# Kernel optimization log

Hardware: AMD Instinct MI355X
Metric: run time of the kernel (lower is better)

## Reference

```python
import jax, jax.numpy as jnp
import numpy as np

B, L = 128, 64000
FS, STEP, NFILT, HID, HID2, OUT = 256, 200, 64, 512, 512, 10


def _ilin(lb, ub, W, b=0.0):
    # interval affine: center/radius form
    c = (lb + ub) * 0.5
    r = (ub - lb) * 0.5
    oc = c @ W + b
    orr = r @ jnp.abs(W)
    return oc - orr, oc + orr


def _imul(al, au, bl, bu):
    # interval product: extremes over 4 corner products
    p = jnp.stack([al * bl, al * bu, au * bl, au * bu])
    return p.min(axis=0), p.max(axis=0)


def _cell(xl, xu, hl, hu, cl, cu, wih, whh, bias):
    # interval LSTM cell, torch gate order i,f,g,o
    gl1, gu1 = _ilin(xl, xu, wih)
    gl2, gu2 = _ilin(hl, hu, whh)
    gl = gl1 + gl2 + bias
    gu = gu1 + gu2 + bias
    il, fl, ggl, ol = jnp.split(gl, 4, axis=-1)
    iu, fu, ggu, ou = jnp.split(gu, 4, axis=-1)
    il, iu = jax.nn.sigmoid(il), jax.nn.sigmoid(iu)
    fl, fu = jax.nn.sigmoid(fl), jax.nn.sigmoid(fu)
    ggl, ggu = jnp.tanh(ggl), jnp.tanh(ggu)
    fcl, fcu = _imul(fl, fu, cl, cu)
    igl, igu = _imul(il, iu, ggl, ggu)
    ncl, ncu = fcl + igl, fcu + igu
    nhl, nhu = _imul(jax.nn.sigmoid(ol), jax.nn.sigmoid(ou), jnp.tanh(ncl), jnp.tanh(ncu))
    return nhl, nhu, ncl, ncu


def setup_inputs() -> dict:
    key = jax.random.key(0)
    ks = jax.random.split(key, 13)
    x = 0.1 * jax.random.normal(ks[0], (B, L), jnp.float32)
    eps = 0.01
    s = 0.3  # keep LSTM gates out of saturation
    return {
        "input_lb": x - eps,
        "input_ub": x + eps,
        "mtx1": jax.random.normal(ks[1], (FS, FS + 2), jnp.float32) / np.float32(np.sqrt(FS)),
        "mtx2": jax.random.uniform(ks[2], (FS + 2, NFILT), jnp.float32) / np.float32(FS + 2),
        "lin1_w": jax.random.normal(ks[3], (NFILT, HID), jnp.float32) / np.float32(np.sqrt(NFILT)),
        "lin1_b": 0.01 * jax.random.normal(ks[4], (HID,), jnp.float32),
        "w_ih0": s * jax.random.normal(ks[5], (HID, 4 * HID2), jnp.float32) / np.float32(np.sqrt(HID)),
        "w_hh0": s * jax.random.normal(ks[6], (HID2, 4 * HID2), jnp.float32) / np.float32(np.sqrt(HID2)),
        "b0": 0.01 * jax.random.normal(ks[7], (4 * HID2,), jnp.float32),
        "w_ih1": s * jax.random.normal(ks[8], (HID2, 4 * HID2), jnp.float32) / np.float32(np.sqrt(HID2)),
        "w_hh1": s * jax.random.normal(ks[9], (HID2, 4 * HID2), jnp.float32) / np.float32(np.sqrt(HID2)),
        "b1": 0.01 * jax.random.normal(ks[10], (4 * HID2,), jnp.float32),
        "lin2_w": jax.random.normal(ks[11], (HID2, OUT), jnp.float32) / np.float32(np.sqrt(HID2)),
        "lin2_b": 0.01 * jax.random.normal(ks[12], (OUT,), jnp.float32),
    }


def reference(input_lb, input_ub, mtx1, mtx2, lin1_w, lin1_b,
              w_ih0, w_hh0, b0, w_ih1, w_hh1, b1, lin2_w, lin2_b):
    Bc, Lc = input_lb.shape
    pad = jnp.zeros((Bc, STEP), input_lb.dtype)
    lb = jnp.concatenate([input_lb, pad], axis=1)
    ub = jnp.concatenate([input_ub, pad], axis=1)
    Lp = Lc + STEP
    F = (Lp - FS - 1) // STEP + 1  # frames with i + FS < Lp (break condition)
    idx = jnp.arange(F)[:, None] * STEP + jnp.arange(FS)[None, :]  # [F, FS]
    flb, fub = lb[:, idx], ub[:, idx]  # [B, F, FS]
    # pre-LSTM interval chain, vectorized over all frames
    l1l, l1u = _ilin(flb, fub, mtx1)  # [B, F, FS+2]
    a, b = l1l * l1l, l1u * l1u
    squ = jnp.maximum(a, b)
    sql = jnp.where((l1l <= 0) & (l1u >= 0), 0.0, jnp.minimum(a, b))
    l2l, l2u = _ilin(sql, squ, mtx2, 1e-10)  # mtx2 >= 0, inputs >= 0 -> lb > 0
    lgl, lgu = jnp.log(l2l), jnp.log(l2u)
    n1l, n1u = _ilin(lgl, lgu, lin1_w, lin1_b)  # [B, F, HID]
    rl, ru = jnp.maximum(n1l, 0.0), jnp.maximum(n1u, 0.0)

    H2 = w_hh0.shape[0]
    z = jnp.zeros((Bc, H2), input_lb.dtype)

    def step(carry, xs):
        h0l, h0u, c0l, c0u, h1l, h1u, c1l, c1u = carry
        xl, xu = xs
        h0l, h0u, c0l, c0u = _cell(xl, xu, h0l, h0u, c0l, c0u, w_ih0, w_hh0, b0)
        h1l, h1u, c1l, c1u = _cell(h0l, h0u, h1l, h1u, c1l, c1u, w_ih1, w_hh1, b1)
        return (h0l, h0u, c0l, c0u, h1l, h1u, c1l, c1u), None

    carry, _ = jax.lax.scan(step, (z,) * 8,
                            (jnp.swapaxes(rl, 0, 1), jnp.swapaxes(ru, 0, 1)))
    h1l, h1u = carry[4], carry[5]  # last frame, top LSTM layer
    ol, ou = _ilin(h1l, h1u, lin2_w, lin2_b)
    return jnp.stack([ol, ou])  # [2, B, OUT] logit bounds
```

## Files before the change

kernel.cpp:

```cpp
#include <hip/hip_runtime.h>
#include <hip/hip_bf16.h>
#include <math.h>

#define BATCH 128
#define LEN   64000
#define FS    256
#define STEPS 200
#define NFILT 64
#define HID   512
#define HID2  512
#define NOUT  10
#define NF    320
#define G4    2048
#define KTOT  1024
#define NBLK  256
#define HSLOT (BATCH * HID2)

typedef __bf16  bf16x8 __attribute__((ext_vector_type(8)));
typedef float   f32x4  __attribute__((ext_vector_type(4)));
typedef __hip_bfloat16 hbf;

#define ARV(b)  (128 + (b) * 16)
#define REL_(i) (128 + 4096 + (i) * 16)
#define BAR_WORDS (128 + 4096 + 128)

__device__ __forceinline__ float fsig(float x) { return 1.f / (1.f + __expf(-x)); }
__device__ __forceinline__ float ftanh(float x) { return 1.f - 2.f / (__expf(2.f * x) + 1.f); }
__device__ __forceinline__ void imulf_(float al, float au, float bl, float bu,
                                       float& lo, float& hi) {
    const float p1 = al * bl, p2 = al * bu, p3 = au * bl, p4 = au * bu;
    lo = fminf(fminf(p1, p2), fminf(p3, p4));
    hi = fmaxf(fmaxf(p1, p2), fmaxf(p3, p4));
}

__device__ __forceinline__ bf16x8 loadA16_agent(const hbf* p) {
    union { unsigned long long u[2]; bf16x8 v; } t;
    unsigned long long* q = (unsigned long long*)p;
    t.u[0] = __hip_atomic_load(q,     __ATOMIC_RELAXED, __HIP_MEMORY_SCOPE_AGENT);
    t.u[1] = __hip_atomic_load(q + 1, __ATOMIC_RELAXED, __HIP_MEMORY_SCOPE_AGENT);
    return t.v;
}
__device__ __forceinline__ unsigned ld_flag(const unsigned* p) {
    return __hip_atomic_load(p, __ATOMIC_RELAXED, __HIP_MEMORY_SCOPE_AGENT);
}
__device__ __forceinline__ void st_flag(unsigned* p, unsigned v) {
    __hip_atomic_store(p, v, __ATOMIC_RELAXED, __HIP_MEMORY_SCOPE_AGENT);
}

__global__ __launch_bounds__(256) void prep_weights_kernel(
    const float* __restrict__ wih, const float* __restrict__ whh,
    hbf* __restrict__ Wt)
{
    __shared__ float tile[32][33];
    const int n0 = blockIdx.x * 32;
    const int k0 = blockIdx.y * 32;
    const int tx = threadIdx.x & 31;
    const int ty = threadIdx.x >> 5;

    for (int r = ty; r < 32; r += 8) {
        const int k = k0 + r;
        const float* src = (k < HID) ? (wih + (size_t)k * G4)
                                     : (whh + (size_t)(k - HID) * G4);
        tile[r][tx] = src[n0 + tx];
    }
    __syncthreads();
    for (int r = ty; r < 32; r += 8) {
        const int n = n0 + r;
        Wt[(size_t)n * KTOT + k0 + tx] = __float2bfloat16(tile[tx][r]);
    }
}

__global__ __launch_bounds__(256) void prep_mtx1_kernel(
    const float* __restrict__ mtx1, hbf* __restrict__ W)
{
    __shared__ float tile[32][33];
    const int n0 = blockIdx.x * 32;
    const int k0 = blockIdx.y * 32;
    const int tx = threadIdx.x & 31;
    const int ty = threadIdx.x >> 5;

    for (int r = ty; r < 32; r += 8) {
        const int k = k0 + r;
        const int n = n0 + tx;
        tile[r][tx] = (n < FS + 2) ? mtx1[k * (FS + 2) + n] : 0.f;
    }
    __syncthreads();
    for (int r = ty; r < 32; r += 8) {
        const int n = n0 + r;
        if (n < 272)
            W[(size_t)n * 256 + k0 + tx] = __float2bfloat16(tile[tx][r]);
    }
}

__global__ __launch_bounds__(256) void prep_lin1_kernel(
    const float* __restrict__ lin1_w, hbf* __restrict__ W)
{
    __shared__ float tile[32][33];
    const int n0 = blockIdx.x * 32;
    const int k0 = blockIdx.y * 32;
    const int tx = threadIdx.x & 31;
    const int ty = threadIdx.x >> 5;

    for (int r = ty; r < 32; r += 8)
        tile[r][tx] = lin1_w[(size_t)(k0 + r) * HID + n0 + tx];
    __syncthreads();
    for (int r = ty; r < 32; r += 8)
        W[(size_t)(n0 + r) * 64 + k0 + tx] = __float2bfloat16(tile[tx][r]);
}

#define FB_A1C  0
#define FB_A1R  8704
#define FB_O1C  17408
#define FB_O1R  34816
#define FB_S3C  52224
#define FB_S3R  54272
#define FB_SIZE 56320

__global__ __launch_bounds__(512) void frontend3_kernel(
    const float* __restrict__ lb, const float* __restrict__ ub,
    const hbf* __restrict__ Wt1f,
    const float* __restrict__ mtx2,
    const hbf* __restrict__ Wt3f,
    const float* __restrict__ lin1_b,
    hbf* __restrict__ Xc, hbf* __restrict__ Xr)
{
    __shared__ char fbuf[FB_SIZE];
    hbf*   A1c = (hbf*)(fbuf + FB_A1C);
    hbf*   A1r = (hbf*)(fbuf + FB_A1R);
    float* o1C = (float*)(fbuf + FB_O1C);
    float* o1R = (float*)(fbuf + FB_O1R);
    hbf*   SQL = A1c;
    hbf*   SQU = A1r;
    hbf*   s3c = (hbf*)(fbuf + FB_S3C);
    hbf*   s3r = (hbf*)(fbuf + FB_S3R);

    const int tid  = threadIdx.x;
    const int row0 = blockIdx.x * 16;
    const int b    = row0 / NF;
    const int f0   = row0 % NF;

    for (int c = tid; c < 16 * 256; c += 512) {
        const int m = c >> 8, i = c & 255;
        const int pos = (f0 + m) * STEPS + i;
        float l = 0.f, u = 0.f;
        if (pos < LEN) {
            l = lb[(size_t)b * LEN + pos];
            u = ub[(size_t)b * LEN + pos];
        }
        A1c[m * 272 + i] = __float2bfloat16(0.5f * (l + u));
        A1r[m * 272 + i] = __float2bfloat16(0.5f * (u - l));
    }
    __syncthreads();

    {
        const int w    = tid >> 6;
        const int lane = tid & 63;
        const int op   = w & 1;
        const int nh   = w >> 1;
        const int rc   = lane & 15;
        const int gk   = lane >> 4;
        const unsigned amask = op ? 0x7FFF7FFFu : 0xFFFFFFFFu;
        const hbf* ap = (op ? A1r : A1c) + rc * 272 + 8 * gk;
        float* outp = op ? o1R : o1C;
        const int nt0 = nh * 4, nt1 = (nh == 3) ? 17 : nh * 4 + 4;

        for (int nt = nt0; nt < nt1; ++nt) {
            f32x4 acc = {0.f, 0.f, 0.f, 0.f};
            const hbf* bp = Wt1f + (size_t)(nt * 16 + rc) * 256 + 8 * gk;
#pragma unroll
            for (int k0 = 0; k0 < 256; k0 += 32) {
                const bf16x8 afr = *(const bf16x8*)(ap + k0);
                union { bf16x8 v; unsigned u[4]; } t2;
                t2.v = *(const bf16x8*)(bp + k0);
                t2.u[0] &= amask; t2.u[1] &= amask;
                t2.u[2] &= amask; t2.u[3] &= amask;
                acc = __builtin_amdgcn_mfma_f32_16x16x32_bf16(afr, t2.v, acc, 0, 0, 0);
            }
            const int n = nt * 16 + rc;
#pragma unroll
            for (int reg = 0; reg < 4; ++reg)
                outp[(4 * gk + reg) * 272 + n] = acc[reg];
        }
    }
    __syncthreads();

    for (int c = tid; c < 16 * 258; c += 512) {
        const int m = c / 258, n = c - m * 258;
        const float oc = o1C[m * 272 + n];
        const float orr = o1R[m * 272 + n];
        const float l1l = oc - orr, l1u = oc + orr;
        const float a = l1l * l1l, bb = l1u * l1u;
        const float squ = fmaxf(a, bb);
        const float sql = (l1l <= 0.f && l1u >= 0.f) ? 0.f : fminf(a, bb);
        SQL[m * 272 + n] = __float2bfloat16(sql);
        SQU[m * 272 + n] = __float2bfloat16(squ);
    }
    __syncthreads();

    for (int idx = tid; idx < 16 * 64; idx += 512) {
        const int m = idx >> 6, n = idx & 63;
        float l2l = 1e-10f, l2u = 1e-10f;
#pragma unroll 2
        for (int i = 0; i < 258; ++i) {
            const float w = mtx2[i * NFILT + n];
            l2l = fmaf(__bfloat162float(SQL[m * 272 + i]), w, l2l);
            l2u = fmaf(__bfloat162float(SQU[m * 272 + i]), w, l2u);
        }
        const float lgl = logf(l2l);
        const float lgu = logf(l2u);
        s3c[m * 64 + n] = __float2bfloat16(0.5f * (lgl + lgu));
        s3r[m * 64 + n] = __float2bfloat16(0.5f * (lgu - lgl));
    }
    __syncthreads();

    {
        const int w    = tid >> 6;
        const int lane = tid & 63;
        const int rc   = lane & 15;
        const int gk   = lane >> 4;
        const hbf* apc = s3c + rc * 64 + 8 * gk;
        const hbf* apr = s3r + rc * 64 + 8 * gk;

        for (int nt = w * 4; nt < w * 4 + 4; ++nt) {
            f32x4 accC = {0.f, 0.f, 0.f, 0.f};
            f32x4 accR = {0.f, 0.f, 0.f, 0.f};
            const hbf* bp = Wt3f + (size_t)(nt * 16 + rc) * 64 + 8 * gk;
#pragma unroll
            for (int k0 = 0; k0 < 64; k0 += 32) {
                const bf16x8 ac = *(const bf16x8*)(apc + k0);
                const bf16x8 ar = *(const bf16x8*)(apr + k0);
                union { bf16x8 v; unsigned u[4]; } tw, ta;
                tw.v = *(const bf16x8*)(bp + k0);
                ta.v = tw.v;
                ta.u[0] &= 0x7FFF7FFFu; ta.u[1] &= 0x7FFF7FFFu;
                ta.u[2] &= 0x7FFF7FFFu; ta.u[3] &= 0x7FFF7FFFu;
                accC = __builtin_amdgcn_mfma_f32_16x16x32_bf16(ac, tw.v, accC, 0, 0, 0);
                accR = __builtin_amdgcn_mfma_f32_16x16x32_bf16(ar, ta.v, accR, 0, 0, 0);
            }
            const int n = nt * 16 + rc;
            const float bn = lin1_b[n];
#pragma unroll
            for (int reg = 0; reg < 4; ++reg) {
                const int m = 4 * gk + reg;
                const float oc = accC[reg] + bn;
                const float orr = accR[reg];
                const float n1l = oc - orr, n1u = oc + orr;
                const float rl = fmaxf(n1l, 0.f), ru = fmaxf(n1u, 0.f);
                const size_t o = ((size_t)(f0 + m) * BATCH + b) * HID + n;
                Xc[o] = __float2bfloat16(0.5f * (rl + ru));
                Xr[o] = __float2bfloat16(0.5f * (ru - rl));
            }
        }
    }
}

__device__ __forceinline__ void gbar(unsigned* bar, unsigned gen,
                                     int bid, int tid) {
    __builtin_amdgcn_s_waitcnt(0);
    __syncthreads();
    if (bid == 0) {
        if (tid != 0) {
            while (ld_flag(&bar[ARV(tid)]) < gen)
                __builtin_amdgcn_s_sleep(1);
        }
        __syncthreads();
        if (tid < 8) st_flag(&bar[REL_(tid)], gen);
    } else {
        if (tid == 0) {
            st_flag(&bar[ARV(bid)], gen);
            while (ld_flag(&bar[REL_(bid & 7)]) < gen)
                __builtin_amdgcn_s_sleep(4);
        }
        asm volatile("" ::: "memory");
    }
    __syncthreads();
}

__device__ __forceinline__ void cell_elem(
    const float C[4], const float R[4], const float bs[4],
    float& cl_r, float& cu_r, float& nhl, float& nhu)
{
    float gl[4], gu[4];
#pragma unroll
    for (int g = 0; g < 4; ++g) {
        gl[g] = C[g] - R[g] + bs[g];
        gu[g] = C[g] + R[g] + bs[g];
    }
    const float il = fsig(gl[0]), iu = fsig(gu[0]);
    const float fl = fsig(gl[1]), fu = fsig(gu[1]);
    const float ggl = ftanh(gl[2]), ggu = ftanh(gu[2]);
    const float ol = fsig(gl[3]), ou = fsig(gu[3]);

    float fcl, fcu, igl, igu;
    imulf_(fl, fu, cl_r, cu_r, fcl, fcu);
    imulf_(il, iu, ggl, ggu, igl, igu);
    const float ncl = fcl + igl, ncu = fcu + igu;
    cl_r = ncl; cu_r = ncu;
    imulf_(ol, ou, ftanh(ncl), ftanh(ncu), nhl, nhu);
}

#define GEMM_HALF(KBASE, MASKED)                                               \
    _Pragma("unroll")                                                          \
    for (int kk = 0; kk < 16; ++kk) {                                          \
        const int KK = (KBASE) + kk;                                           \
        _Pragma("unroll")                                                      \
        for (int g = 0; g < 4; ++g) {                                          \
            union { bf16x8 v; unsigned u[4]; } t2;                             \
            t2.v = *(const bf16x8*)&Wlds[(size_t)(((g << 5) | KK) * 64 + lane) * 8]; \
            if (MASKED) {                                                      \
                t2.u[0] &= 0x7FFF7FFFu; t2.u[1] &= 0x7FFF7FFFu;                \
                t2.u[2] &= 0x7FFF7FFFu; t2.u[3] &= 0x7FFF7FFFu;                \
            }                                                                  \
            acc[g] = __builtin_amdgcn_mfma_f32_16x16x32_bf16(af[kk], t2.v, acc[g], 0, 0, 0); \
        }                                                                      \
    }

#define LOADA16(PTR)                                                           \
    _Pragma("unroll")                                                          \
    for (int i = 0; i < 16; ++i) af[i] = *(const bf16x8*)((PTR) + 32 * i);

#define POLL_GROUP(BASE, TGT)                                                  \
    if (tid < 64) {                                                            \
        const unsigned* pp = &lflags[((BASE) + (tid & 31)) * 16];              \
        for (;;) {                                                             \
            const unsigned v = ld_flag(pp);                                    \
            if (__all((int)v >= (TGT))) break;                                 \
            __builtin_amdgcn_s_sleep(1);                                       \
        }                                                                      \
    }                                                                          \
    __syncthreads();

__global__ __launch_bounds__(256, 1) void lstm_persistent(
    const hbf* Xc, const hbf* Xr,
    hbf* Ring1C, hbf* Ring1R,
    const hbf* __restrict__ Wt0, const hbf* __restrict__ Wt1,
    const float* __restrict__ b0, const float* __restrict__ b1,
    hbf* __restrict__ Ring0C, hbf* __restrict__ Ring0R,
    const hbf* __restrict__ Zbuf,
    hbf* __restrict__ H1c0, hbf* __restrict__ H1r0,
    hbf* __restrict__ H1c1, hbf* __restrict__ H1r1,
    float* __restrict__ h1l, float* __restrict__ h1u,
    unsigned* __restrict__ bar, unsigned* __restrict__ tkt,
    unsigned* __restrict__ lflags)
{
    const int tid = threadIdx.x;
    const int bid = blockIdx.x;

    __shared__ unsigned s_info, s_map;
    __shared__ int s_fast;
    __shared__ hbf   Wlds[4 * 32 * 64 * 8];
    __shared__ float red[2][2][4][64][4];
    __shared__ unsigned short houtC[32][16], houtR[32][16];

    if (tid == 0) {
        unsigned xcc;
        asm volatile("s_getreg_b32 %0, hwreg(HW_REG_XCC_ID)" : "=s"(xcc));
        xcc &= 7u;
        const unsigned slot = __hip_atomic_fetch_add(
            &tkt[xcc * 16], 1u, __ATOMIC_RELAXED, __HIP_MEMORY_SCOPE_AGENT);
        s_info = (xcc << 16) | slot;
    }
    gbar(bar, 1, bid, tid);
    if (tid == 0) {
        unsigned cnt[8]; bool ok = true;
        for (int y = 0; y < 8; ++y) {
            cnt[y] = ld_flag(&tkt[y * 16]);
            ok = ok && (cnt[y] == 32u);
        }
        const unsigned xcc = s_info >> 16, slot = s_info & 0xffffu;
        unsigned rank;
        if (ok) rank = xcc * 32u + slot;
        else { rank = slot; for (unsigned y = 0; y < xcc; ++y) rank += cnt[y]; }
        s_map = rank; s_fast = ok ? 1 : 0;
    }
    __syncthreads();

    const unsigned rank = s_map;
    const bool fast = (s_fast != 0);
    int layer, mgrp, jslot;
    if (fast) { layer = (rank >> 5) & 1; mgrp = rank >> 6; jslot = rank & 31; }
    else      { layer = rank >> 7; mgrp = (rank >> 5) & 3; jslot = rank & 31; }
    const int m0 = mgrp * 32;
    const int j0 = jslot * 16;
    const int lfbase  = layer * 128 + mgrp * 32;
    const int l0fbase = mgrp * 32;
    const int myLf = lfbase + jslot;

    {
        const hbf* Wt = layer ? Wt1 : Wt0;
        for (int c = tid; c < 8192; c += 256) {
            const int g  = c >> 11;
            const int kk = (c >> 6) & 31;
            const int l6 = c & 63;
            const int n  = g * HID2 + j0 + (l6 & 15);
            const int k  = kk * 32 + (l6 >> 4) * 8;
            *(ulonglong2*)&Wlds[(size_t)c * 8] =
                *(const ulonglong2*)(Wt + (size_t)n * KTOT + k);
        }
    }

    const int w    = tid >> 6;
    const int lane = tid & 63;
    const int op   = w & 1;
    const int mh   = w >> 1;
    const int rc   = lane & 15;
    const int gk   = lane >> 4;
    const int aoff = (m0 + mh * 16 + rc) * 512 + 8 * gk;

    hbf* H1cb[2] = { H1c0, H1c1 };
    hbf* H1rb[2] = { H1r0, H1r1 };

    const int mm  = tid >> 4;
    const int cj  = tid & 15;
    const int ll  = ((mm >> 2) << 4) | cj;
    const int rr  = mm & 3;
    const int idx0 = (m0 + mm) * HID2 + j0 + cj;
    const int idx1 = idx0 + 16 * HID2;
    const float* bias = layer ? b1 : b0;
    float bs[4];
#pragma unroll
    for (int g = 0; g < 4; ++g) bs[g] = bias[g * HID2 + j0 + cj];

    const int st_arr = tid >> 7;
    const int st_row = (tid >> 2) & 31;
    const int st_q   = tid & 3;
    const size_t st_off = (size_t)(m0 + st_row) * 512 + j0 + st_q * 4;

    float cAl = 0.f, cAu = 0.f, cBl = 0.f, cBu = 0.f;

    __syncthreads();

    bf16x8 xf[16];
    if (layer == 0) {
        const hbf* p = (op ? Xr : Xc) + aoff;
        bf16x8* af = xf;
        LOADA16(p)
    }

    for (int t = 0; t < NF; ++t) {
        const int wslot = t & 1, rslot = wslot ^ 1;
        f32x4 acc[4] = {f32x4{0,0,0,0}, f32x4{0,0,0,0},
                        f32x4{0,0,0,0}, f32x4{0,0,0,0}};

        if (layer == 0) {
            {
                bf16x8* af = xf;
                if (op) { GEMM_HALF(0, 1) } else { GEMM_HALF(0, 0) }
                const int tn = (t + 1 < NF) ? (t + 1) : t;
                const hbf* p = (op ? Xr : Xc) + (size_t)tn * HSLOT + aoff;
                LOADA16(p)
            }
            POLL_GROUP(lfbase, t)
            {
                const int pt = (t == 0) ? NF : t - 1;
                const hbf* p = (op ? Ring0R : Ring0C) + (size_t)pt * HSLOT + aoff;
                bf16x8 af[16];
                LOADA16(p)
                if (op) { GEMM_HALF(16, 1) } else { GEMM_HALF(16, 0) }
            }
        } else {
            POLL_GROUP(lfbase, t)
            {
                bf16x8 af[16];
                if (fast) {
                    const hbf* p = (t == 0) ? (Zbuf + aoff)
                        : ((op ? (const hbf*)Ring1R : (const hbf*)Ring1C)
                           + (size_t)(t - 1) * HSLOT + aoff);
                    LOADA16(p)
                } else {
                    const hbf* p = (op ? H1rb[rslot] : H1cb[rslot]) + aoff;
#pragma unroll
                    for (int i = 0; i < 16; ++i) af[i] = loadA16_agent(p + 32 * i);
                }
                if (op) { GEMM_HALF(16, 1) } else { GEMM_HALF(16, 0) }
            }
            POLL_GROUP(l0fbase, t + 1)
            {
                const hbf* p = (op ? Ring0R : Ring0C) + (size_t)t * HSLOT + aoff;
                bf16x8 af[16];
                LOADA16(p)
                if (op) { GEMM_HALF(0, 1) } else { GEMM_HALF(0, 0) }
            }
        }

#pragma unroll
        for (int g = 0; g < 4; ++g)
            *((f32x4*)&red[op][mh][g][lane][0]) = acc[g];
        __syncthreads();

        {
            float C0[4], R0[4], C1[4], R1[4];
#pragma unroll
            for (int g = 0; g < 4; ++g) {
                C0[g] = red[0][0][g][ll][rr];
                R0[g] = red[1][0][g][ll][rr];
                C1[g] = red[0][1][g][ll][rr];
                R1[g] = red[1][1][g][ll][rr];
            }
            const bool writeF = (layer == 1) && (t == NF - 1);

            float nhl, nhu;
            cell_elem(C0, R0, bs, cAl, cAu, nhl, nhu);
            {
                const __hip_bfloat16 hc = __float2bfloat16(0.5f * (nhl + nhu));
                const __hip_bfloat16 hr = __float2bfloat16(0.5f * (nhu - nhl));
                houtC[mm][cj] = *(const unsigned short*)&hc;
                houtR[mm][cj] = *(const unsigned short*)&hr;
            }
            if (writeF) { h1l[idx0] = nhl; h1u[idx0] = nhu; }

            cell_elem(C1, R1, bs, cBl, cBu, nhl, nhu);
            {
                const __hip_bfloat16 hc = __float2bfloat16(0.5f * (nhl + nhu));
                const __hip_bfloat16 hr = __float2bfloat16(0.5f * (nhu - nhl));
                houtC[mm + 16][cj] = *(const unsigned short*)&hc;
                houtR[mm + 16][cj] = *(const unsigned short*)&hr;
            }
            if (writeF) { h1l[idx1] = nhl; h1u[idx1] = nhu; }
        }
        __syncthreads();

        {
            hbf *dstC, *dstR;
            if (layer == 0) {
                dstC = Ring0C + (size_t)t * HSLOT;
                dstR = Ring0R + (size_t)t * HSLOT;
            } else if (fast) {
                dstC = Ring1C + (size_t)t * HSLOT;
                dstR = Ring1R + (size_t)t * HSLOT;
            } else {
                dstC = H1cb[wslot];
                dstR = H1rb[wslot];
            }
            const unsigned long long* src = (const unsigned long long*)
                &(st_arr ? houtR : houtC)[st_row][st_q * 4];
            unsigned long long* dst = (unsigned long long*)
                ((st_arr ? dstR : dstC) + st_off);
            __hip_atomic_store(dst, *src, __ATOMIC_RELAXED,
                               __HIP_MEMORY_SCOPE_AGENT);
        }

        __builtin_amdgcn_s_waitcnt(0);
        __syncthreads();
        if (tid == 0)
            st_flag(&lflags[myLf * 16], (unsigned)(t + 1));
    }
}

__global__ __launch_bounds__(64) void final_kernel(
    const float* __restrict__ h1l, const float* __restrict__ h1u,
    const float* __restrict__ w, const float* __restrict__ bias,
    float* __restrict__ out)
{
    const int b = blockIdx.x;
    const int j = threadIdx.x;
    if (j < NOUT) {
        float oc = bias[j], orr = 0.f;
        for (int i = 0; i < HID2; ++i) {
            const float lo = h1l[(size_t)b * HID2 + i];
            const float hi = h1u[(size_t)b * HID2 + i];
            const float wv = w[i * NOUT + j];
            oc  = fmaf(0.5f * (lo + hi), wv, oc);
            orr = fmaf(0.5f * (hi - lo), fabsf(wv), orr);
        }
        out[b * NOUT + j] = oc - orr;
        out[BATCH * NOUT + b * NOUT + j] = oc + orr;
    }
}

extern "C" void kernel_launch(void* const* d_in, const int* in_sizes, int n_in,
                              void* d_out, int out_size, void* d_ws, size_t ws_size,
                              hipStream_t stream)
{
    const float* input_lb = (const float*)d_in[0];
    const float* input_ub = (const float*)d_in[1];
    const float* mtx1     = (const float*)d_in[2];
    const float* mtx2     = (const float*)d_in[3];
    const float* lin1_w   = (const float*)d_in[4];
    const float* lin1_b   = (const float*)d_in[5];
    const float* w_ih0    = (const float*)d_in[6];
    const float* w_hh0    = (const float*)d_in[7];
    const float* b0       = (const float*)d_in[8];
    const float* w_ih1    = (const float*)d_in[9];
    const float* w_hh1    = (const float*)d_in[10];
    const float* b1       = (const float*)d_in[11];
    const float* lin2_w   = (const float*)d_in[12];
    const float* lin2_b   = (const float*)d_in[13];
    float* out = (float*)d_out;

    char* ws = (char*)d_ws;
    size_t off = 0;
    hbf* Xc = (hbf*)(ws + off); off += (size_t)NF * HSLOT * 2;
    hbf* Xr = (hbf*)(ws + off); off += (size_t)NF * HSLOT * 2;
    hbf* Wt0 = (hbf*)(ws + off); off += (size_t)G4 * KTOT * 2;
    hbf* Wt1 = (hbf*)(ws + off); off += (size_t)G4 * KTOT * 2;
    hbf* Wt1f = (hbf*)(ws + off); off += (size_t)272 * 256 * 2;
    hbf* Wt3f = (hbf*)(ws + off); off += (size_t)512 * 64 * 2;
    hbf* Ring0C = (hbf*)(ws + off); off += (size_t)(NF + 1) * HSLOT * 2;
    hbf* Ring0R = (hbf*)(ws + off); off += (size_t)(NF + 1) * HSLOT * 2;

    char* zbase = ws + off;
    hbf* Zbuf = (hbf*)(ws + off); off += (size_t)HSLOT * 2;
    hbf* H1c0 = (hbf*)(ws + off); off += (size_t)HSLOT * 2;
    hbf* H1r0 = (hbf*)(ws + off); off += (size_t)HSLOT * 2;
    hbf* H1c1 = (hbf*)(ws + off); off += (size_t)HSLOT * 2;
    hbf* H1r1 = (hbf*)(ws + off); off += (size_t)HSLOT * 2;
    unsigned* lflags = (unsigned*)(ws + off); off += (size_t)256 * 16 * 4;
    unsigned* tkt    = (unsigned*)(ws + off); off += (size_t)8 * 16 * 4;
    unsigned* bar    = (unsigned*)(ws + off); off += (size_t)BAR_WORDS * 4;
    const size_t zbytes = (size_t)((ws + off) - zbase);
    float* h1l = (float*)(ws + off); off += (size_t)HSLOT * 4;
    float* h1u = (float*)(ws + off); off += (size_t)HSLOT * 4;

    hipMemsetAsync(zbase, 0, zbytes, stream);
    hipMemsetAsync(Ring0C + (size_t)NF * HSLOT, 0, (size_t)HSLOT * 2, stream);
    hipMemsetAsync(Ring0R + (size_t)NF * HSLOT, 0, (size_t)HSLOT * 2, stream);

    {
        const dim3 pgrid(G4 / 32, KTOT / 32);
        prep_weights_kernel<<<pgrid, 256, 0, stream>>>(w_ih0, w_hh0, Wt0);
        prep_weights_kernel<<<pgrid, 256, 0, stream>>>(w_ih1, w_hh1, Wt1);
        prep_mtx1_kernel<<<dim3(9, 8), 256, 0, stream>>>(mtx1, Wt1f);
        prep_lin1_kernel<<<dim3(16, 2), 256, 0, stream>>>(lin1_w, Wt3f);
    }

    frontend3_kernel<<<(BATCH * NF) / 16, 512, 0, stream>>>(
        input_lb, input_ub, Wt1f, mtx2, Wt3f, lin1_b, Xc, Xr);

    lstm_persistent<<<NBLK, 256, 0, stream>>>(
        Xc, Xr, Xc, Xr, Wt0, Wt1, b0, b1,
        Ring0C, Ring0R, Zbuf,
        H1c0, H1r0, H1c1, H1r1,
        h1l, h1u, bar, tkt, lflags);

    final_kernel<<<BATCH, 64, 0, stream>>>(h1l, h1u, lin2_w, lin2_b, out);
}
```

Baseline: 2.911 ms.

## Replace per-block flag polling with group atomic counters and private layer-0 ring copy

Each block used to publish its own per-step flag, and consumers polled 32 flags with a full wavefront. Now each block does an atomic add on a shared per-group counter, and one thread polls it until it reaches 32*t. Layer-0 outputs are also written, with plain stores, to a second ring that only layer-0 readers use, so their reads do not contend with the layer-1 consumers. The t==0 case now reads a zero buffer instead of a padded ring slot. This trades the flag polling for atomic contention on one counter and for extra write traffic and workspace, and the extra ring is used only if the workspace is large enough.

```diff
diff --git a/kernel.cpp b/kernel.cpp
--- a/kernel.cpp
+++ b/kernel.cpp
@@ -19,6 +19,7 @@
 typedef __bf16  bf16x8 __attribute__((ext_vector_type(8)));
 typedef float   f32x4  __attribute__((ext_vector_type(4)));
 typedef __hip_bfloat16 hbf;
+typedef unsigned long long ull;
 
 #define ARV(b)  (128 + (b) * 16)
 #define REL_(i) (128 + 4096 + (i) * 16)
@@ -34,8 +35,8 @@
 }
 
 __device__ __forceinline__ bf16x8 loadA16_agent(const hbf* p) {
-    union { unsigned long long u[2]; bf16x8 v; } t;
-    unsigned long long* q = (unsigned long long*)p;
+    union { ull u[2]; bf16x8 v; } t;
+    ull* q = (ull*)p;
     t.u[0] = __hip_atomic_load(q,     __ATOMIC_RELAXED, __HIP_MEMORY_SCOPE_AGENT);
     t.u[1] = __hip_atomic_load(q + 1, __ATOMIC_RELAXED, __HIP_MEMORY_SCOPE_AGENT);
     return t.v;
@@ -319,14 +320,10 @@
     _Pragma("unroll")                                                          \
     for (int i = 0; i < 16; ++i) af[i] = *(const bf16x8*)((PTR) + 32 * i);
 
-#define POLL_GROUP(BASE, TGT)                                                  \
-    if (tid < 64) {                                                            \
-        const unsigned* pp = &lflags[((BASE) + (tid & 31)) * 16];              \
-        for (;;) {                                                             \
-            const unsigned v = ld_flag(pp);                                    \
-            if (__all((int)v >= (TGT))) break;                                 \
-            __builtin_amdgcn_s_sleep(1);                                       \
-        }                                                                      \
+#define POLL_CNT(GID, TGT)                                                     \
+    if (tid == 0) {                                                            \
+        const unsigned* pp = &gcnt[(GID) * 16];                                \
+        while ((int)ld_flag(pp) < (TGT)) __builtin_amdgcn_s_sleep(1);          \
     }                                                                          \
     __syncthreads();
 
@@ -336,12 +333,14 @@
     const hbf* __restrict__ Wt0, const hbf* __restrict__ Wt1,
     const float* __restrict__ b0, const float* __restrict__ b1,
     hbf* __restrict__ Ring0C, hbf* __restrict__ Ring0R,
+    hbf* __restrict__ RP0C, hbf* __restrict__ RP0R,
+    int useP0,
     const hbf* __restrict__ Zbuf,
     hbf* __restrict__ H1c0, hbf* __restrict__ H1r0,
     hbf* __restrict__ H1c1, hbf* __restrict__ H1r1,
     float* __restrict__ h1l, float* __restrict__ h1u,
     unsigned* __restrict__ bar, unsigned* __restrict__ tkt,
-    unsigned* __restrict__ lflags)
+    unsigned* __restrict__ gcnt)
 {
     const int tid = threadIdx.x;
     const int bid = blockIdx.x;
@@ -382,9 +381,9 @@
     else      { layer = rank >> 7; mgrp = (rank >> 5) & 3; jslot = rank & 31; }
     const int m0 = mgrp * 32;
     const int j0 = jslot * 16;
-    const int lfbase  = layer * 128 + mgrp * 32;
-    const int l0fbase = mgrp * 32;
-    const int myLf = lfbase + jslot;
+    const int gid  = layer * 4 + mgrp;
+    const int pgid = mgrp;
+    const bool p0 = fast && (useP0 != 0);
 
     {
         const hbf* Wt = layer ? Wt1 : Wt0;
@@ -450,16 +449,18 @@
                 const hbf* p = (op ? Xr : Xc) + (size_t)tn * HSLOT + aoff;
                 LOADA16(p)
             }
-            POLL_GROUP(lfbase, t)
+            POLL_CNT(gid, 32 * t)
             {
-                const int pt = (t == 0) ? NF : t - 1;
-                const hbf* p = (op ? Ring0R : Ring0C) + (size_t)pt * HSLOT + aoff;
+                const hbf* p;
+                if (t == 0)       p = Zbuf + aoff;
+                else if (p0)      p = (op ? RP0R : RP0C) + (size_t)(t - 1) * HSLOT + aoff;
+                else              p = (op ? Ring0R : Ring0C) + (size_t)(t - 1) * HSLOT + aoff;
                 bf16x8 af[16];
                 LOADA16(p)
                 if (op) { GEMM_HALF(16, 1) } else { GEMM_HALF(16, 0) }
             }
         } else {
-            POLL_GROUP(lfbase, t)
+            POLL_CNT(gid, 32 * t)
             {
                 bf16x8 af[16];
                 if (fast) {
@@ -474,7 +475,7 @@
                 }
                 if (op) { GEMM_HALF(16, 1) } else { GEMM_HALF(16, 0) }
             }
-            POLL_GROUP(l0fbase, t + 1)
+            POLL_CNT(pgid, 32 * (t + 1))
             {
                 const hbf* p = (op ? Ring0R : Ring0C) + (size_t)t * HSLOT + aoff;
                 bf16x8 af[16];
@@ -521,29 +522,35 @@
         __syncthreads();
 
         {
-            hbf *dstC, *dstR;
+            const ull v = *(const ull*)
+                &(st_arr ? houtR : houtC)[st_row][st_q * 4];
             if (layer == 0) {
-                dstC = Ring0C + (size_t)t * HSLOT;
-                dstR = Ring0R + (size_t)t * HSLOT;
+                hbf* aC = Ring0C + (size_t)t * HSLOT;
+                hbf* aR = Ring0R + (size_t)t * HSLOT;
+                __hip_atomic_store((ull*)((st_arr ? aR : aC) + st_off), v,
+                                   __ATOMIC_RELAXED, __HIP_MEMORY_SCOPE_AGENT);
+                if (p0) {
+                    hbf* pC = RP0C + (size_t)t * HSLOT;
+                    hbf* pR = RP0R + (size_t)t * HSLOT;
+                    *(ull*)((st_arr ? pR : pC) + st_off) = v;
+                }
             } else if (fast) {
-                dstC = Ring1C + (size_t)t * HSLOT;
-                dstR = Ring1R + (size_t)t * HSLOT;
+                hbf* pC = Ring1C + (size_t)t * HSLOT;
+                hbf* pR = Ring1R + (size_t)t * HSLOT;
+                *(ull*)((st_arr ? pR : pC) + st_off) = v;
             } else {
-                dstC = H1cb[wslot];
-                dstR = H1rb[wslot];
-            }
-            const unsigned long long* src = (const unsigned long long*)
-                &(st_arr ? houtR : houtC)[st_row][st_q * 4];
-            unsigned long long* dst = (unsigned long long*)
-                ((st_arr ? dstR : dstC) + st_off);
-            __hip_atomic_store(dst, *src, __ATOMIC_RELAXED,
-                               __HIP_MEMORY_SCOPE_AGENT);
+                hbf* dC = H1cb[wslot];
+                hbf* dR = H1rb[wslot];
+                __hip_atomic_store((ull*)((st_arr ? dR : dC) + st_off), v,
+                                   __ATOMIC_RELAXED, __HIP_MEMORY_SCOPE_AGENT);
+            }
         }
 
         __builtin_amdgcn_s_waitcnt(0);
         __syncthreads();
         if (tid == 0)
-            st_flag(&lflags[myLf * 16], (unsigned)(t + 1));
+            __hip_atomic_fetch_add(&gcnt[gid * 16], 1u, __ATOMIC_RELAXED,
+                                   __HIP_MEMORY_SCOPE_AGENT);
     }
 }
 
@@ -596,8 +603,8 @@
     hbf* Wt1 = (hbf*)(ws + off); off += (size_t)G4 * KTOT * 2;
     hbf* Wt1f = (hbf*)(ws + off); off += (size_t)272 * 256 * 2;
     hbf* Wt3f = (hbf*)(ws + off); off += (size_t)512 * 64 * 2;
-    hbf* Ring0C = (hbf*)(ws + off); off += (size_t)(NF + 1) * HSLOT * 2;
-    hbf* Ring0R = (hbf*)(ws + off); off += (size_t)(NF + 1) * HSLOT * 2;
+    hbf* Ring0C = (hbf*)(ws + off); off += (size_t)NF * HSLOT * 2;
+    hbf* Ring0R = (hbf*)(ws + off); off += (size_t)NF * HSLOT * 2;
 
     char* zbase = ws + off;
     hbf* Zbuf = (hbf*)(ws + off); off += (size_t)HSLOT * 2;
@@ -605,16 +612,26 @@
     hbf* H1r0 = (hbf*)(ws + off); off += (size_t)HSLOT * 2;
     hbf* H1c1 = (hbf*)(ws + off); off += (size_t)HSLOT * 2;
     hbf* H1r1 = (hbf*)(ws + off); off += (size_t)HSLOT * 2;
-    unsigned* lflags = (unsigned*)(ws + off); off += (size_t)256 * 16 * 4;
-    unsigned* tkt    = (unsigned*)(ws + off); off += (size_t)8 * 16 * 4;
-    unsigned* bar    = (unsigned*)(ws + off); off += (size_t)BAR_WORDS * 4;
+    unsigned* tkt  = (unsigned*)(ws + off); off += (size_t)8 * 16 * 4;
+    unsigned* bar  = (unsigned*)(ws + off); off += (size_t)BAR_WORDS * 4;
+    unsigned* gcnt = (unsigned*)(ws + off); off += (size_t)8 * 16 * 4;
     const size_t zbytes = (size_t)((ws + off) - zbase);
     float* h1l = (float*)(ws + off); off += (size_t)HSLOT * 4;
     float* h1u = (float*)(ws + off); off += (size_t)HSLOT * 4;
 
+    hbf* RP0C = Ring0C;
+    hbf* RP0R = Ring0R;
+    int useP0 = 0;
+    {
+        const size_t need = (size_t)NF * HSLOT * 2 * 2;
+        if (off + need <= ws_size) {
+            RP0C = (hbf*)(ws + off); off += (size_t)NF * HSLOT * 2;
+            RP0R = (hbf*)(ws + off); off += (size_t)NF * HSLOT * 2;
+            useP0 = 1;
+        }
+    }
+
     hipMemsetAsync(zbase, 0, zbytes, stream);
-    hipMemsetAsync(Ring0C + (size_t)NF * HSLOT, 0, (size_t)HSLOT * 2, stream);
-    hipMemsetAsync(Ring0R + (size_t)NF * HSLOT, 0, (size_t)HSLOT * 2, stream);
 
     {
         const dim3 pgrid(G4 / 32, KTOT / 32);
@@ -629,9 +646,9 @@
 
     lstm_persistent<<<NBLK, 256, 0, stream>>>(
         Xc, Xr, Xc, Xr, Wt0, Wt1, b0, b1,
-        Ring0C, Ring0R, Zbuf,
+        Ring0C, Ring0R, RP0C, RP0R, useP0, Zbuf,
         H1c0, H1r0, H1c1, H1r1,
-        h1l, h1u, bar, tkt, lflags);
+        h1l, h1u, bar, tkt, gcnt);
 
     final_kernel<<<BATCH, 64, 0, stream>>>(h1l, h1u, lin2_w, lin2_b, out);
 }
```

Result: faster. 2.794 ms, median of 2 (-4.0%).
